# Kernel optimization log

Measured on AMD Instinct MI355X. Metric: run time of the kernel, lower is better.

Reference implementation:

```python
import jax, jax.numpy as jnp
import numpy as np


def _linear_interp(t, S):
    """1D linear interpolation along last axis, matching F.interpolate(mode='linear', align_corners=False).
    t: [B, C, L] -> [B, C, S]"""
    L = t.shape[-1]
    src = jnp.clip((jnp.arange(S, dtype=jnp.float32) + 0.5) * (L / S) - 0.5, 0.0, L - 1)
    i0 = jnp.floor(src).astype(jnp.int32)
    i1 = jnp.minimum(i0 + 1, L - 1)
    w = (src - i0.astype(jnp.float32)).astype(t.dtype)
    return t[..., i0] * (1.0 - w) + t[..., i1] * w


def setup_inputs() -> dict:
    key = jax.random.key(0)
    k1, k2, k3, k4 = jax.random.split(key, 4)
    B, C, H, W, L, D = 32, 768, 32, 32, 77, 512
    return {
        "img_feat": jax.random.normal(k1, (B, C, H, W), dtype=jnp.float32),
        "text_feat": jax.random.normal(k2, (B, L, D), dtype=jnp.float32),
        "W_txt": jax.random.normal(k3, (D, C), dtype=jnp.float32) / np.float32(np.sqrt(D)),
        "gamma": jax.random.normal(k4, (1,), dtype=jnp.float32) * 0.1,
    }


def reference(img_feat, text_feat, W_txt, gamma):
    B, C, H, W = img_feat.shape
    S = H * W
    q = img_feat.reshape(B, C, S)                          # [B,C,S]
    # Linear(D->C, bias=False) then transpose(1,2): [B,L,D] -> [B,C,L]
    t = jnp.einsum('bld,dc->bcl', text_feat, W_txt)
    t = _linear_interp(t, S)                               # [B,C,S]
    scale = S ** (-0.5)
    # attn = bmm(q [B,C,S], t^T [B,S,C]) * scale -> [B,C,C] channel attention
    attn = jax.nn.softmax(jnp.einsum('bis,bjs->bij', q, t) * scale, axis=-1)
    out = q + gamma * jnp.einsum('bij,bjs->bis', attn, t)  # gamma-gated residual
    return out.reshape(B, C, H, W)
```

## Files before the change

kernel.cpp:

```cpp
#include <hip/hip_runtime.h>

#define BB 32
#define CC 768
#define SS 1024
#define LLn 77
#define DD 512
#define LP 80
#define LP2 96

#define RATIO 0.0751953125f
#define IRATIO 13.298701f

#define CVT_TXT_BLOCKS (BB * LP * DD / 4 / 256)
#define CVT_W_BLOCKS ((CC / 32) * (DD / 32))
#define TG_BLOCKS (BB * 5 * 4)
#define QH_BLOCKS (256 * BB)

typedef short bf16x8 __attribute__((ext_vector_type(8)));
typedef float f32x4 __attribute__((ext_vector_type(4)));
typedef unsigned short u16;

__device__ __forceinline__ u16 f2bf(float f) {
    unsigned int u; __builtin_memcpy(&u, &f, 4);
    u += 0x7fffu + ((u >> 16) & 1u);
    return (u16)(u >> 16);
}

__global__ __launch_bounds__(256) void k_cvt(const float* __restrict__ text,
                                             const float* __restrict__ Wt,
                                             u16* __restrict__ At,
                                             u16* __restrict__ Wb) {
    __shared__ float tile[32 * 33];
    const int bx = blockIdx.x;
    const int tid = threadIdx.x;
    if (bx < CVT_TXT_BLOCKS) {
        int j = bx * 256 + tid;
        int row80 = j >> 7, col4 = (j & 127) << 2;
        int b = row80 / LP, l = row80 - b * LP;
        u16 o[4] = {0, 0, 0, 0};
        if (l < LLn) {
            float4 v = *reinterpret_cast<const float4*>(&text[((size_t)b * LLn + l) * DD + col4]);
            o[0] = f2bf(v.x); o[1] = f2bf(v.y); o[2] = f2bf(v.z); o[3] = f2bf(v.w);
        }
        *reinterpret_cast<uint2*>(&At[(size_t)row80 * DD + col4]) = *reinterpret_cast<uint2*>(o);
    } else {
        const int bw = bx - CVT_TXT_BLOCKS;
        const int c0 = (bw % (CC / 32)) * 32, d0 = (bw / (CC / 32)) * 32;
        const int tx = tid & 31, ty = tid >> 5;
#pragma unroll
        for (int k = 0; k < 4; ++k) {
            int d = ty + k * 8;
            tile[d * 33 + tx] = Wt[(size_t)(d0 + d) * CC + c0 + tx];
        }
        __syncthreads();
#pragma unroll
        for (int k = 0; k < 4; ++k) {
            int c = ty + k * 8;
            Wb[(size_t)(c0 + c) * DD + d0 + tx] = f2bf(tile[tx * 33 + c]);
        }
    }
}

__global__ __launch_bounds__(256) void k_mid(const float* __restrict__ q,
                                             const u16* __restrict__ At,
                                             const u16* __restrict__ Wb,
                                             u16* __restrict__ qh,
                                             u16* __restrict__ tc,
                                             u16* __restrict__ tlc) {
    __shared__ float smem[3 * 1024];
    const int bx = blockIdx.x;
    const int tid = threadIdx.x;

    if (bx < TG_BLOCKS) {
        const int cg = bx / 160, mt = bx % 160;
        const int b = mt / 5, tile = mt % 5;
        const int l0 = tile * 16;
        const int w = tid >> 6, lane = tid & 63;
        const int lm = lane & 15, lg = lane >> 4;
        const int c0 = cg * 192 + w * 48;

        f32x4 acc[3];
#pragma unroll
        for (int nt = 0; nt < 3; ++nt) acc[nt] = (f32x4){0.f, 0.f, 0.f, 0.f};

        const u16* ap = At + ((size_t)b * LP + l0 + lm) * DD + lg * 8;
        const u16* bp = Wb + (size_t)(c0 + lm) * DD + lg * 8;
#pragma unroll 4
        for (int ks = 0; ks < 16; ++ks) {
            bf16x8 aq = *reinterpret_cast<const bf16x8*>(ap + ks * 32);
#pragma unroll
            for (int nt = 0; nt < 3; ++nt) {
                bf16x8 bv = *reinterpret_cast<const bf16x8*>(bp + (size_t)nt * 16 * DD + ks * 32);
                acc[nt] = __builtin_amdgcn_mfma_f32_16x16x32_bf16(aq, bv, acc[nt], 0, 0, 0);
            }
        }

        const int lq = l0 + lg * 4;
#pragma unroll
        for (int nt = 0; nt < 3; ++nt) {
            int c = c0 + nt * 16 + lm;
            u16 pk[4];
#pragma unroll
            for (int r = 0; r < 4; ++r) pk[r] = f2bf(acc[nt][r]);
            uint2 pv; __builtin_memcpy(&pv, pk, 8);
            *reinterpret_cast<uint2*>(&tc[((size_t)b * CC + c) * LP2 + lq]) = pv;
#pragma unroll
            for (int r = 0; r < 4; ++r)
                tlc[((size_t)b * LP + lq + r) * CC + c] = pk[r];
        }
        if (tile == 4 && lg == 0) {
            uint4 z = {0u, 0u, 0u, 0u};
#pragma unroll
            for (int nt = 0; nt < 3; ++nt) {
                int c = c0 + nt * 16 + lm;
                *reinterpret_cast<uint4*>(&tc[((size_t)b * CC + c) * LP2 + 80]) = z;
                *reinterpret_cast<uint4*>(&tc[((size_t)b * CC + c) * LP2 + 88]) = z;
            }
        }
    } else {
        const int bxq = bx - TG_BLOCKS;
        const int b = bxq >> 8;
        const int c0 = (bxq & 255) * 3;
        for (int i4 = tid; i4 < 3 * 256; i4 += 256) {
            int r = i4 >> 8, col = (i4 & 255) << 2;
            *reinterpret_cast<float4*>(&smem[r * 1024 + col]) =
                *reinterpret_cast<const float4*>(&q[((size_t)b * CC + c0 + r) * SS + col]);
        }
        __syncthreads();
        for (int idx = tid; idx < 3 * LP2; idx += 256) {
            int r = idx / LP2, l = idx % LP2;
            float val = 0.f;
            if (l < LLn) {
                int s_lo = max(0, (int)floorf(((float)l - 0.5f) * IRATIO - 0.5f) - 1);
                int s_hi = min(SS - 1, (int)ceilf(((float)l + 1.5f) * IRATIO - 0.5f) + 1);
                float fl = (float)l;
                float a = 0.f;
                for (int s = s_lo; s <= s_hi; ++s) {
                    float src = fmaf((float)s + 0.5f, RATIO, -0.5f);
                    src = fminf(fmaxf(src, 0.f), 76.f);
                    float wgt = fmaxf(0.f, 1.f - fabsf(src - fl));
                    a = fmaf(wgt, smem[r * 1024 + s], a);
                }
                val = a * 0.03125f;
            }
            qh[((size_t)b * CC + c0 + r) * LP2 + l] = f2bf(val);
        }
    }
}

__global__ __launch_bounds__(256, 2) void k_attn_out(const u16* __restrict__ qh,
                                                     const u16* __restrict__ tc,
                                                     const u16* __restrict__ tlc,
                                                     const float* __restrict__ q,
                                                     const float* __restrict__ gamma,
                                                     float* __restrict__ out) {
    __shared__ float pmax[4][16];
    __shared__ float psum[4][16];
    __shared__ float us[16 * 80];
    __shared__ __align__(16) char pbuf[4][6400];

    const int b = blockIdx.y;
    const int iBase = blockIdx.x * 16;
    const int tid = threadIdx.x;
    const int w = tid >> 6, lane = tid & 63;
    const int lm = lane & 15, lg = lane >> 4;
    const float g = gamma[0];

    const u16* qbase = qh + ((size_t)b * CC + iBase + lm) * LP2 + lg * 8;
    bf16x8 aq0 = *reinterpret_cast<const bf16x8*>(qbase);
    bf16x8 aq1 = *reinterpret_cast<const bf16x8*>(qbase + 32);
    bf16x8 aq2 = *reinterpret_cast<const bf16x8*>(qbase + 64);

    f32x4 acc[12];
#pragma unroll
    for (int t = 0; t < 12; ++t) acc[t] = (f32x4){0.f, 0.f, 0.f, 0.f};

    const u16* tcb = tc + ((size_t)b * CC + w * 192 + lm) * LP2 + lg * 8;
#pragma unroll
    for (int t = 0; t < 12; ++t) {
        const u16* p = tcb + (size_t)t * 16 * LP2;
        bf16x8 b0 = *reinterpret_cast<const bf16x8*>(p);
        bf16x8 b1 = *reinterpret_cast<const bf16x8*>(p + 32);
        bf16x8 b2 = *reinterpret_cast<const bf16x8*>(p + 64);
        acc[t] = __builtin_amdgcn_mfma_f32_16x16x32_bf16(aq0, b0, acc[t], 0, 0, 0);
        acc[t] = __builtin_amdgcn_mfma_f32_16x16x32_bf16(aq1, b1, acc[t], 0, 0, 0);
        acc[t] = __builtin_amdgcn_mfma_f32_16x16x32_bf16(aq2, b2, acc[t], 0, 0, 0);
    }

    const size_t qBase = ((size_t)b * CC + iBase) * SS + (size_t)(tid << 2);
    f32x4 qreg[16];
#pragma unroll
    for (int r = 0; r < 16; ++r)
        qreg[r] = *reinterpret_cast<const f32x4*>(&q[qBase + (size_t)r * SS]);

    float m[4];
#pragma unroll
    for (int r = 0; r < 4; ++r) {
        float mm = acc[0][r];
#pragma unroll
        for (int t = 1; t < 12; ++t) mm = fmaxf(mm, acc[t][r]);
#pragma unroll
        for (int off = 8; off >= 1; off >>= 1) mm = fmaxf(mm, __shfl_xor(mm, off));
        m[r] = mm;
    }
    if (lm == 0) {
#pragma unroll
        for (int r = 0; r < 4; ++r) pmax[w][lg * 4 + r] = m[r];
    }
    __syncthreads();
    float gm[4];
#pragma unroll
    for (int r = 0; r < 4; ++r) {
        int row = lg * 4 + r;
        gm[r] = fmaxf(fmaxf(pmax[0][row], pmax[1][row]), fmaxf(pmax[2][row], pmax[3][row]));
    }
    float s[4] = {0.f, 0.f, 0.f, 0.f};
#pragma unroll
    for (int t = 0; t < 12; ++t) {
#pragma unroll
        for (int r = 0; r < 4; ++r) {
            float e = __expf(acc[t][r] - gm[r]);
            acc[t][r] = e;
            s[r] += e;
        }
    }
#pragma unroll
    for (int r = 0; r < 4; ++r) {
#pragma unroll
        for (int off = 8; off >= 1; off >>= 1) s[r] += __shfl_xor(s[r], off);
    }
    if (lm == 0) {
#pragma unroll
        for (int r = 0; r < 4; ++r) psum[w][lg * 4 + r] = s[r];
    }

    u16* P = (u16*)pbuf[w];
#pragma unroll
    for (int t = 0; t < 12; ++t) {
#pragma unroll
        for (int r = 0; r < 4; ++r)
            P[(lg * 4 + r) * 200 + t * 16 + lm] = f2bf(acc[t][r]);
    }

    f32x4 u[5];
#pragma unroll
    for (int nt = 0; nt < 5; ++nt) u[nt] = (f32x4){0.f, 0.f, 0.f, 0.f};
    const u16* tb = tlc + ((size_t)b * LP + lm) * CC + w * 192 + lg * 8;
#pragma unroll
    for (int ks = 0; ks < 6; ++ks) {
        bf16x8 pa = *reinterpret_cast<const bf16x8*>(&P[lm * 200 + ks * 32 + lg * 8]);
#pragma unroll
        for (int nt = 0; nt < 5; ++nt) {
            bf16x8 bv = *reinterpret_cast<const bf16x8*>(tb + (size_t)nt * 16 * CC + ks * 32);
            u[nt] = __builtin_amdgcn_mfma_f32_16x16x32_bf16(pa, bv, u[nt], 0, 0, 0);
        }
    }

    float* up = (float*)pbuf[w];
#pragma unroll
    for (int nt = 0; nt < 5; ++nt) {
#pragma unroll
        for (int r = 0; r < 4; ++r)
            up[(lg * 4 + r) * 81 + nt * 16 + lm] = u[nt][r];
    }
    __syncthreads();
#pragma unroll
    for (int k = 0; k < 5; ++k) {
        int idx = tid + (k << 8);
        int row = idx / LP, l = idx % LP;
        float v = ((float*)pbuf[0])[row * 81 + l] + ((float*)pbuf[1])[row * 81 + l]
                + ((float*)pbuf[2])[row * 81 + l] + ((float*)pbuf[3])[row * 81 + l];
        float denom = psum[0][row] + psum[1][row] + psum[2][row] + psum[3][row];
        us[row * LP + l] = v / denom;
    }
    __syncthreads();

    const int s0 = tid << 2;
    int i0x[4], i1x[4];
    float wx[4];
#pragma unroll
    for (int k = 0; k < 4; ++k) {
        float src = fmaf((float)(s0 + k) + 0.5f, RATIO, -0.5f);
        src = fminf(fmaxf(src, 0.f), 76.f);
        i0x[k] = (int)src;
        wx[k] = src - (float)i0x[k];
        i1x[k] = (i0x[k] < 76) ? i0x[k] + 1 : 76;
    }
#pragma unroll
    for (int r = 0; r < 16; ++r) {
        const float* ur = &us[r * LP];
        f32x4 o;
#pragma unroll
        for (int k = 0; k < 4; ++k) {
            float uv = fmaf(1.f - wx[k], ur[i0x[k]], wx[k] * ur[i1x[k]]);
            o[k] = qreg[r][k] + g * uv;
        }
        __builtin_nontemporal_store(o, reinterpret_cast<f32x4*>(&out[qBase + (size_t)r * SS]));
    }
}

extern "C" void kernel_launch(void* const* d_in, const int* in_sizes, int n_in,
                              void* d_out, int out_size, void* d_ws, size_t ws_size,
                              hipStream_t stream) {
    const float* img   = (const float*)d_in[0];
    const float* text  = (const float*)d_in[1];
    const float* Wt    = (const float*)d_in[2];
    const float* gamma = (const float*)d_in[3];
    float* out = (float*)d_out;
    char* ws = (char*)d_ws;
    u16*   tc_bf  = (u16*)(ws);
    u16*   tlc_bf = (u16*)(ws + 4718592);
    u16*   qh_bf  = (u16*)(ws + 8650752);
    u16*   At_bf  = (u16*)(ws + 13369344);
    u16*   Wb_bf  = (u16*)(ws + 15990784);

    k_cvt<<<dim3(CVT_TXT_BLOCKS + CVT_W_BLOCKS), 256, 0, stream>>>(text, Wt, At_bf, Wb_bf);
    k_mid<<<dim3(TG_BLOCKS + QH_BLOCKS), 256, 0, stream>>>(img, At_bf, Wb_bf, qh_bf, tc_bf, tlc_bf);
    k_attn_out<<<dim3(48, BB), 256, 0, stream>>>(qh_bf, tc_bf, tlc_bf, img, gamma, out);
}
```

Before: 100.3 us.

## Fuse q-side interpolation reduction into attention kernel, dropping separate qh pass

The projection of q onto the 77 text positions (the transpose of the linear interpolation) is now computed inside the attention kernel from the q rows it already loads, using shared-memory atomic accumulation, instead of a separate pass over all of img_feat in the middle kernel. This removes one full read of the 100MB input and the qh round trip through global memory. In exchange it adds shared-memory atomics and extra syncs before the MFMA stage, and the q register loads now come before the score computation.

```diff
diff --git a/kernel.cpp b/kernel.cpp
--- a/kernel.cpp
+++ b/kernel.cpp
@@ -9,12 +9,10 @@
 #define LP2 96
 
 #define RATIO 0.0751953125f
-#define IRATIO 13.298701f
 
 #define CVT_TXT_BLOCKS (BB * LP * DD / 4 / 256)
 #define CVT_W_BLOCKS ((CC / 32) * (DD / 32))
 #define TG_BLOCKS (BB * 5 * 4)
-#define QH_BLOCKS (256 * BB)
 
 typedef short bf16x8 __attribute__((ext_vector_type(8)));
 typedef float f32x4 __attribute__((ext_vector_type(4)));
@@ -61,101 +59,68 @@
     }
 }
 
-__global__ __launch_bounds__(256) void k_mid(const float* __restrict__ q,
-                                             const u16* __restrict__ At,
-                                             const u16* __restrict__ Wb,
-                                             u16* __restrict__ qh,
-                                             u16* __restrict__ tc,
-                                             u16* __restrict__ tlc) {
-    __shared__ float smem[3 * 1024];
+__global__ __launch_bounds__(256) void k_tgemm(const u16* __restrict__ At,
+                                               const u16* __restrict__ Wb,
+                                               u16* __restrict__ tc,
+                                               u16* __restrict__ tlc) {
     const int bx = blockIdx.x;
     const int tid = threadIdx.x;
-
-    if (bx < TG_BLOCKS) {
-        const int cg = bx / 160, mt = bx % 160;
-        const int b = mt / 5, tile = mt % 5;
-        const int l0 = tile * 16;
-        const int w = tid >> 6, lane = tid & 63;
-        const int lm = lane & 15, lg = lane >> 4;
-        const int c0 = cg * 192 + w * 48;
-
-        f32x4 acc[3];
-#pragma unroll
-        for (int nt = 0; nt < 3; ++nt) acc[nt] = (f32x4){0.f, 0.f, 0.f, 0.f};
-
-        const u16* ap = At + ((size_t)b * LP + l0 + lm) * DD + lg * 8;
-        const u16* bp = Wb + (size_t)(c0 + lm) * DD + lg * 8;
+    const int cg = bx / 160, mt = bx % 160;
+    const int b = mt / 5, tile = mt % 5;
+    const int l0 = tile * 16;
+    const int w = tid >> 6, lane = tid & 63;
+    const int lm = lane & 15, lg = lane >> 4;
+    const int c0 = cg * 192 + w * 48;
+
+    f32x4 acc[3];
+#pragma unroll
+    for (int nt = 0; nt < 3; ++nt) acc[nt] = (f32x4){0.f, 0.f, 0.f, 0.f};
+
+    const u16* ap = At + ((size_t)b * LP + l0 + lm) * DD + lg * 8;
+    const u16* bp = Wb + (size_t)(c0 + lm) * DD + lg * 8;
 #pragma unroll 4
-        for (int ks = 0; ks < 16; ++ks) {
-            bf16x8 aq = *reinterpret_cast<const bf16x8*>(ap + ks * 32);
-#pragma unroll
-            for (int nt = 0; nt < 3; ++nt) {
-                bf16x8 bv = *reinterpret_cast<const bf16x8*>(bp + (size_t)nt * 16 * DD + ks * 32);
-                acc[nt] = __builtin_amdgcn_mfma_f32_16x16x32_bf16(aq, bv, acc[nt], 0, 0, 0);
-            }
-        }
-
-        const int lq = l0 + lg * 4;
+    for (int ks = 0; ks < 16; ++ks) {
+        bf16x8 aq = *reinterpret_cast<const bf16x8*>(ap + ks * 32);
+#pragma unroll
+        for (int nt = 0; nt < 3; ++nt) {
+            bf16x8 bv = *reinterpret_cast<const bf16x8*>(bp + (size_t)nt * 16 * DD + ks * 32);
+            acc[nt] = __builtin_amdgcn_mfma_f32_16x16x32_bf16(aq, bv, acc[nt], 0, 0, 0);
+        }
+    }
+
+    const int lq = l0 + lg * 4;
+#pragma unroll
+    for (int nt = 0; nt < 3; ++nt) {
+        int c = c0 + nt * 16 + lm;
+        u16 pk[4];
+#pragma unroll
+        for (int r = 0; r < 4; ++r) pk[r] = f2bf(acc[nt][r]);
+        uint2 pv; __builtin_memcpy(&pv, pk, 8);
+        *reinterpret_cast<uint2*>(&tc[((size_t)b * CC + c) * LP2 + lq]) = pv;
+#pragma unroll
+        for (int r = 0; r < 4; ++r)
+            tlc[((size_t)b * LP + lq + r) * CC + c] = pk[r];
+    }
+    if (tile == 4 && lg == 0) {
+        uint4 z = {0u, 0u, 0u, 0u};
 #pragma unroll
         for (int nt = 0; nt < 3; ++nt) {
             int c = c0 + nt * 16 + lm;
-            u16 pk[4];
-#pragma unroll
-            for (int r = 0; r < 4; ++r) pk[r] = f2bf(acc[nt][r]);
-            uint2 pv; __builtin_memcpy(&pv, pk, 8);
-            *reinterpret_cast<uint2*>(&tc[((size_t)b * CC + c) * LP2 + lq]) = pv;
-#pragma unroll
-            for (int r = 0; r < 4; ++r)
-                tlc[((size_t)b * LP + lq + r) * CC + c] = pk[r];
-        }
-        if (tile == 4 && lg == 0) {
-            uint4 z = {0u, 0u, 0u, 0u};
-#pragma unroll
-            for (int nt = 0; nt < 3; ++nt) {
-                int c = c0 + nt * 16 + lm;
-                *reinterpret_cast<uint4*>(&tc[((size_t)b * CC + c) * LP2 + 80]) = z;
-                *reinterpret_cast<uint4*>(&tc[((size_t)b * CC + c) * LP2 + 88]) = z;
-            }
-        }
-    } else {
-        const int bxq = bx - TG_BLOCKS;
-        const int b = bxq >> 8;
-        const int c0 = (bxq & 255) * 3;
-        for (int i4 = tid; i4 < 3 * 256; i4 += 256) {
-            int r = i4 >> 8, col = (i4 & 255) << 2;
-            *reinterpret_cast<float4*>(&smem[r * 1024 + col]) =
-                *reinterpret_cast<const float4*>(&q[((size_t)b * CC + c0 + r) * SS + col]);
-        }
-        __syncthreads();
-        for (int idx = tid; idx < 3 * LP2; idx += 256) {
-            int r = idx / LP2, l = idx % LP2;
-            float val = 0.f;
-            if (l < LLn) {
-                int s_lo = max(0, (int)floorf(((float)l - 0.5f) * IRATIO - 0.5f) - 1);
-                int s_hi = min(SS - 1, (int)ceilf(((float)l + 1.5f) * IRATIO - 0.5f) + 1);
-                float fl = (float)l;
-                float a = 0.f;
-                for (int s = s_lo; s <= s_hi; ++s) {
-                    float src = fmaf((float)s + 0.5f, RATIO, -0.5f);
-                    src = fminf(fmaxf(src, 0.f), 76.f);
-                    float wgt = fmaxf(0.f, 1.f - fabsf(src - fl));
-                    a = fmaf(wgt, smem[r * 1024 + s], a);
-                }
-                val = a * 0.03125f;
-            }
-            qh[((size_t)b * CC + c0 + r) * LP2 + l] = f2bf(val);
-        }
-    }
-}
-
-__global__ __launch_bounds__(256, 2) void k_attn_out(const u16* __restrict__ qh,
-                                                     const u16* __restrict__ tc,
-                                                     const u16* __restrict__ tlc,
-                                                     const float* __restrict__ q,
-                                                     const float* __restrict__ gamma,
-                                                     float* __restrict__ out) {
+            *reinterpret_cast<uint4*>(&tc[((size_t)b * CC + c) * LP2 + 80]) = z;
+            *reinterpret_cast<uint4*>(&tc[((size_t)b * CC + c) * LP2 + 88]) = z;
+        }
+    }
+}
+
+__global__ __launch_bounds__(256, 2) void k_fused(const u16* __restrict__ tc,
+                                                  const u16* __restrict__ tlc,
+                                                  const float* __restrict__ q,
+                                                  const float* __restrict__ gamma,
+                                                  float* __restrict__ out) {
     __shared__ float pmax[4][16];
     __shared__ float psum[4][16];
+    __shared__ float qh_f32[16 * 80];
+    __shared__ u16 qh_bf[16 * 96];
     __shared__ float us[16 * 80];
     __shared__ __align__(16) char pbuf[4][6400];
 
@@ -166,10 +131,53 @@
     const int lm = lane & 15, lg = lane >> 4;
     const float g = gamma[0];
 
-    const u16* qbase = qh + ((size_t)b * CC + iBase + lm) * LP2 + lg * 8;
-    bf16x8 aq0 = *reinterpret_cast<const bf16x8*>(qbase);
-    bf16x8 aq1 = *reinterpret_cast<const bf16x8*>(qbase + 32);
-    bf16x8 aq2 = *reinterpret_cast<const bf16x8*>(qbase + 64);
+    const size_t qBase = ((size_t)b * CC + iBase) * SS + (size_t)(tid << 2);
+    f32x4 qreg[16];
+#pragma unroll
+    for (int r = 0; r < 16; ++r)
+        qreg[r] = *reinterpret_cast<const f32x4*>(&q[qBase + (size_t)r * SS]);
+
+    for (int i = tid; i < 16 * 80; i += 256) qh_f32[i] = 0.f;
+    __syncthreads();
+
+    const int s0 = tid << 2;
+    float wgt[4]; int i0k[4];
+#pragma unroll
+    for (int k = 0; k < 4; ++k) {
+        float src = fmaf((float)(s0 + k) + 0.5f, RATIO, -0.5f);
+        src = fminf(fmaxf(src, 0.f), 76.f);
+        i0k[k] = (int)src;
+        wgt[k] = src - (float)i0k[k];
+    }
+    const int la = i0k[0];
+#pragma unroll
+    for (int r = 0; r < 16; ++r) {
+        float c0 = 0.f, c1 = 0.f, c2 = 0.f;
+#pragma unroll
+        for (int k = 0; k < 4; ++k) {
+            float qv = qreg[r][k];
+            bool hi = (i0k[k] != la);
+            float a0 = (1.f - wgt[k]) * qv, a1 = wgt[k] * qv;
+            c0 += hi ? 0.f : a0;
+            c1 += hi ? a0 : a1;
+            c2 += hi ? a1 : 0.f;
+        }
+        atomicAdd(&qh_f32[r * 80 + la], c0);
+        atomicAdd(&qh_f32[r * 80 + la + 1], c1);
+        if (c2 != 0.f) atomicAdd(&qh_f32[r * 80 + la + 2], c2);
+    }
+    __syncthreads();
+
+    for (int i = tid; i < 16 * 96; i += 256) {
+        int row = i / 96, col = i - row * 96;
+        float v = (col < LLn) ? qh_f32[row * 80 + col] * 0.03125f : 0.f;
+        qh_bf[i] = f2bf(v);
+    }
+    __syncthreads();
+
+    bf16x8 aq0 = *reinterpret_cast<const bf16x8*>(&qh_bf[lm * 96 + lg * 8]);
+    bf16x8 aq1 = *reinterpret_cast<const bf16x8*>(&qh_bf[lm * 96 + 32 + lg * 8]);
+    bf16x8 aq2 = *reinterpret_cast<const bf16x8*>(&qh_bf[lm * 96 + 64 + lg * 8]);
 
     f32x4 acc[12];
 #pragma unroll
@@ -187,12 +195,6 @@
         acc[t] = __builtin_amdgcn_mfma_f32_16x16x32_bf16(aq2, b2, acc[t], 0, 0, 0);
     }
 
-    const size_t qBase = ((size_t)b * CC + iBase) * SS + (size_t)(tid << 2);
-    f32x4 qreg[16];
-#pragma unroll
-    for (int r = 0; r < 16; ++r)
-        qreg[r] = *reinterpret_cast<const f32x4*>(&q[qBase + (size_t)r * SS]);
-
     float m[4];
 #pragma unroll
     for (int r = 0; r < 4; ++r) {
@@ -275,24 +277,16 @@
     }
     __syncthreads();
 
-    const int s0 = tid << 2;
-    int i0x[4], i1x[4];
-    float wx[4];
-#pragma unroll
-    for (int k = 0; k < 4; ++k) {
-        float src = fmaf((float)(s0 + k) + 0.5f, RATIO, -0.5f);
-        src = fminf(fmaxf(src, 0.f), 76.f);
-        i0x[k] = (int)src;
-        wx[k] = src - (float)i0x[k];
-        i1x[k] = (i0x[k] < 76) ? i0x[k] + 1 : 76;
-    }
+    int i1x[4];
+#pragma unroll
+    for (int k = 0; k < 4; ++k) i1x[k] = (i0k[k] < 76) ? i0k[k] + 1 : 76;
 #pragma unroll
     for (int r = 0; r < 16; ++r) {
         const float* ur = &us[r * LP];
         f32x4 o;
 #pragma unroll
         for (int k = 0; k < 4; ++k) {
-            float uv = fmaf(1.f - wx[k], ur[i0x[k]], wx[k] * ur[i1x[k]]);
+            float uv = fmaf(1.f - wgt[k], ur[i0k[k]], wgt[k] * ur[i1x[k]]);
             o[k] = qreg[r][k] + g * uv;
         }
         __builtin_nontemporal_store(o, reinterpret_cast<f32x4*>(&out[qBase + (size_t)r * SS]));
@@ -310,11 +304,10 @@
     char* ws = (char*)d_ws;
     u16*   tc_bf  = (u16*)(ws);
     u16*   tlc_bf = (u16*)(ws + 4718592);
-    u16*   qh_bf  = (u16*)(ws + 8650752);
-    u16*   At_bf  = (u16*)(ws + 13369344);
-    u16*   Wb_bf  = (u16*)(ws + 15990784);
+    u16*   At_bf  = (u16*)(ws + 8650752);
+    u16*   Wb_bf  = (u16*)(ws + 11272192);
 
     k_cvt<<<dim3(CVT_TXT_BLOCKS + CVT_W_BLOCKS), 256, 0, stream>>>(text, Wt, At_bf, Wb_bf);
-    k_mid<<<dim3(TG_BLOCKS + QH_BLOCKS), 256, 0, stream>>>(img, At_bf, Wb_bf, qh_bf, tc_bf, tlc_bf);
-    k_attn_out<<<dim3(48, BB), 256, 0, stream>>>(qh_bf, tc_bf, tlc_bf, img, gamma, out);
-}
+    k_tgemm<<<dim3(TG_BLOCKS), 256, 0, stream>>>(At_bf, Wb_bf, tc_bf, tlc_bf);
+    k_fused<<<dim3(48, BB), 256, 0, stream>>>(tc_bf, tlc_bf, img, gamma, out);
+}
```

After: 168.8 us. +68.3%, slower.

## Rebalance kernel stages and remap attention blocks across batches

Applied to the files above, without the earlier changes.

Moves the q-downsampling work (qh) out of the middle kernel into the first prep kernel alongside the text/weight conversions. This leaves a small dedicated text-GEMM kernel and makes the large q-read pass independent of the GEMM. The attention kernel switches to a 1D grid whose block ids are swizzled so consecutive blocks cover eight different batches, changing which blocks share cache and which XCD each lands on. The risk is that the prep kernel grows and the text GEMM becomes a small, underfilled launch of its own.

```diff
diff --git a/kernel.cpp b/kernel.cpp
--- a/kernel.cpp
+++ b/kernel.cpp
@@ -13,26 +13,34 @@
 
 #define CVT_TXT_BLOCKS (BB * LP * DD / 4 / 256)
 #define CVT_W_BLOCKS ((CC / 32) * (DD / 32))
+#define QH_BLOCKS (256 * BB)
+#define PREP_BLOCKS (CVT_TXT_BLOCKS + CVT_W_BLOCKS + QH_BLOCKS)
 #define TG_BLOCKS (BB * 5 * 4)
-#define QH_BLOCKS (256 * BB)
+#define ATTN_BLOCKS (48 * BB)
 
 typedef short bf16x8 __attribute__((ext_vector_type(8)));
 typedef float f32x4 __attribute__((ext_vector_type(4)));
 typedef unsigned short u16;
+typedef unsigned int u32;
+
+#define MFMA __builtin_amdgcn_mfma_f32_16x16x32_bf16
 
 __device__ __forceinline__ u16 f2bf(float f) {
-    unsigned int u; __builtin_memcpy(&u, &f, 4);
+    u32 u; __builtin_memcpy(&u, &f, 4);
     u += 0x7fffu + ((u >> 16) & 1u);
     return (u16)(u >> 16);
 }
 
-__global__ __launch_bounds__(256) void k_cvt(const float* __restrict__ text,
-                                             const float* __restrict__ Wt,
-                                             u16* __restrict__ At,
-                                             u16* __restrict__ Wb) {
-    __shared__ float tile[32 * 33];
+__global__ __launch_bounds__(256) void k_prep(const float* __restrict__ q,
+                                              const float* __restrict__ text,
+                                              const float* __restrict__ Wt,
+                                              u16* __restrict__ At,
+                                              u16* __restrict__ Wb,
+                                              u16* __restrict__ qh) {
+    __shared__ float smem[3 * 1024];
     const int bx = blockIdx.x;
     const int tid = threadIdx.x;
+
     if (bx < CVT_TXT_BLOCKS) {
         int j = bx * 256 + tid;
         int row80 = j >> 7, col4 = (j & 127) << 2;
@@ -43,10 +51,11 @@
             o[0] = f2bf(v.x); o[1] = f2bf(v.y); o[2] = f2bf(v.z); o[3] = f2bf(v.w);
         }
         *reinterpret_cast<uint2*>(&At[(size_t)row80 * DD + col4]) = *reinterpret_cast<uint2*>(o);
-    } else {
+    } else if (bx < CVT_TXT_BLOCKS + CVT_W_BLOCKS) {
         const int bw = bx - CVT_TXT_BLOCKS;
         const int c0 = (bw % (CC / 32)) * 32, d0 = (bw / (CC / 32)) * 32;
         const int tx = tid & 31, ty = tid >> 5;
+        float* tile = smem;
 #pragma unroll
         for (int k = 0; k < 4; ++k) {
             int d = ty + k * 8;
@@ -58,67 +67,8 @@
             int c = ty + k * 8;
             Wb[(size_t)(c0 + c) * DD + d0 + tx] = f2bf(tile[tx * 33 + c]);
         }
-    }
-}
-
-__global__ __launch_bounds__(256) void k_mid(const float* __restrict__ q,
-                                             const u16* __restrict__ At,
-                                             const u16* __restrict__ Wb,
-                                             u16* __restrict__ qh,
-                                             u16* __restrict__ tc,
-                                             u16* __restrict__ tlc) {
-    __shared__ float smem[3 * 1024];
-    const int bx = blockIdx.x;
-    const int tid = threadIdx.x;
-
-    if (bx < TG_BLOCKS) {
-        const int cg = bx / 160, mt = bx % 160;
-        const int b = mt / 5, tile = mt % 5;
-        const int l0 = tile * 16;
-        const int w = tid >> 6, lane = tid & 63;
-        const int lm = lane & 15, lg = lane >> 4;
-        const int c0 = cg * 192 + w * 48;
-
-        f32x4 acc[3];
-#pragma unroll
-        for (int nt = 0; nt < 3; ++nt) acc[nt] = (f32x4){0.f, 0.f, 0.f, 0.f};
-
-        const u16* ap = At + ((size_t)b * LP + l0 + lm) * DD + lg * 8;
-        const u16* bp = Wb + (size_t)(c0 + lm) * DD + lg * 8;
-#pragma unroll 4
-        for (int ks = 0; ks < 16; ++ks) {
-            bf16x8 aq = *reinterpret_cast<const bf16x8*>(ap + ks * 32);
-#pragma unroll
-            for (int nt = 0; nt < 3; ++nt) {
-                bf16x8 bv = *reinterpret_cast<const bf16x8*>(bp + (size_t)nt * 16 * DD + ks * 32);
-                acc[nt] = __builtin_amdgcn_mfma_f32_16x16x32_bf16(aq, bv, acc[nt], 0, 0, 0);
-            }
-        }
-
-        const int lq = l0 + lg * 4;
-#pragma unroll
-        for (int nt = 0; nt < 3; ++nt) {
-            int c = c0 + nt * 16 + lm;
-            u16 pk[4];
-#pragma unroll
-            for (int r = 0; r < 4; ++r) pk[r] = f2bf(acc[nt][r]);
-            uint2 pv; __builtin_memcpy(&pv, pk, 8);
-            *reinterpret_cast<uint2*>(&tc[((size_t)b * CC + c) * LP2 + lq]) = pv;
-#pragma unroll
-            for (int r = 0; r < 4; ++r)
-                tlc[((size_t)b * LP + lq + r) * CC + c] = pk[r];
-        }
-        if (tile == 4 && lg == 0) {
-            uint4 z = {0u, 0u, 0u, 0u};
-#pragma unroll
-            for (int nt = 0; nt < 3; ++nt) {
-                int c = c0 + nt * 16 + lm;
-                *reinterpret_cast<uint4*>(&tc[((size_t)b * CC + c) * LP2 + 80]) = z;
-                *reinterpret_cast<uint4*>(&tc[((size_t)b * CC + c) * LP2 + 88]) = z;
-            }
-        }
     } else {
-        const int bxq = bx - TG_BLOCKS;
+        const int bxq = bx - CVT_TXT_BLOCKS - CVT_W_BLOCKS;
         const int b = bxq >> 8;
         const int c0 = (bxq & 255) * 3;
         for (int i4 = tid; i4 < 3 * 256; i4 += 256) {
@@ -148,6 +98,59 @@
     }
 }
 
+__global__ __launch_bounds__(256) void k_tgemm(const u16* __restrict__ At,
+                                               const u16* __restrict__ Wb,
+                                               u16* __restrict__ tc,
+                                               u16* __restrict__ tlc) {
+    const int bx = blockIdx.x;
+    const int tid = threadIdx.x;
+    const int cg = bx / 160, mt = bx % 160;
+    const int b = mt / 5, tile = mt % 5;
+    const int l0 = tile * 16;
+    const int w = tid >> 6, lane = tid & 63;
+    const int lm = lane & 15, lg = lane >> 4;
+    const int c0 = cg * 192 + w * 48;
+
+    f32x4 acc[3];
+#pragma unroll
+    for (int nt = 0; nt < 3; ++nt) acc[nt] = (f32x4){0.f, 0.f, 0.f, 0.f};
+
+    const u16* ap = At + ((size_t)b * LP + l0 + lm) * DD + lg * 8;
+    const u16* bp = Wb + (size_t)(c0 + lm) * DD + lg * 8;
+#pragma unroll 4
+    for (int ks = 0; ks < 16; ++ks) {
+        bf16x8 aq = *reinterpret_cast<const bf16x8*>(ap + ks * 32);
+#pragma unroll
+        for (int nt = 0; nt < 3; ++nt) {
+            bf16x8 bv = *reinterpret_cast<const bf16x8*>(bp + (size_t)nt * 16 * DD + ks * 32);
+            acc[nt] = MFMA(aq, bv, acc[nt], 0, 0, 0);
+        }
+    }
+
+    const int lq = l0 + lg * 4;
+#pragma unroll
+    for (int nt = 0; nt < 3; ++nt) {
+        int c = c0 + nt * 16 + lm;
+        u16 pk[4];
+#pragma unroll
+        for (int r = 0; r < 4; ++r) pk[r] = f2bf(acc[nt][r]);
+        uint2 pv; __builtin_memcpy(&pv, pk, 8);
+        *reinterpret_cast<uint2*>(&tc[((size_t)b * CC + c) * LP2 + lq]) = pv;
+#pragma unroll
+        for (int r = 0; r < 4; ++r)
+            tlc[((size_t)b * LP + lq + r) * CC + c] = pk[r];
+    }
+    if (tile == 4 && lg == 0) {
+        uint4 z = {0u, 0u, 0u, 0u};
+#pragma unroll
+        for (int nt = 0; nt < 3; ++nt) {
+            int c = c0 + nt * 16 + lm;
+            *reinterpret_cast<uint4*>(&tc[((size_t)b * CC + c) * LP2 + 80]) = z;
+            *reinterpret_cast<uint4*>(&tc[((size_t)b * CC + c) * LP2 + 88]) = z;
+        }
+    }
+}
+
 __global__ __launch_bounds__(256, 2) void k_attn_out(const u16* __restrict__ qh,
                                                      const u16* __restrict__ tc,
                                                      const u16* __restrict__ tlc,
@@ -159,8 +162,10 @@
     __shared__ float us[16 * 80];
     __shared__ __align__(16) char pbuf[4][6400];
 
-    const int b = blockIdx.y;
-    const int iBase = blockIdx.x * 16;
+    const int id = blockIdx.x;
+    const int o = id >> 3;
+    const int b = (id & 7) * 4 + o / 48;
+    const int iBase = (o % 48) * 16;
     const int tid = threadIdx.x;
     const int w = tid >> 6, lane = tid & 63;
     const int lm = lane & 15, lg = lane >> 4;
@@ -182,9 +187,9 @@
         bf16x8 b0 = *reinterpret_cast<const bf16x8*>(p);
         bf16x8 b1 = *reinterpret_cast<const bf16x8*>(p + 32);
         bf16x8 b2 = *reinterpret_cast<const bf16x8*>(p + 64);
-        acc[t] = __builtin_amdgcn_mfma_f32_16x16x32_bf16(aq0, b0, acc[t], 0, 0, 0);
-        acc[t] = __builtin_amdgcn_mfma_f32_16x16x32_bf16(aq1, b1, acc[t], 0, 0, 0);
-        acc[t] = __builtin_amdgcn_mfma_f32_16x16x32_bf16(aq2, b2, acc[t], 0, 0, 0);
+        acc[t] = MFMA(aq0, b0, acc[t], 0, 0, 0);
+        acc[t] = MFMA(aq1, b1, acc[t], 0, 0, 0);
+        acc[t] = MFMA(aq2, b2, acc[t], 0, 0, 0);
     }
 
     const size_t qBase = ((size_t)b * CC + iBase) * SS + (size_t)(tid << 2);
@@ -252,7 +257,7 @@
 #pragma unroll
         for (int nt = 0; nt < 5; ++nt) {
             bf16x8 bv = *reinterpret_cast<const bf16x8*>(tb + (size_t)nt * 16 * CC + ks * 32);
-            u[nt] = __builtin_amdgcn_mfma_f32_16x16x32_bf16(pa, bv, u[nt], 0, 0, 0);
+            u[nt] = MFMA(pa, bv, u[nt], 0, 0, 0);
         }
     }
 
@@ -267,7 +272,7 @@
 #pragma unroll
     for (int k = 0; k < 5; ++k) {
         int idx = tid + (k << 8);
-        int row = idx / LP, l = idx % LP;
+        int row = idx / LP, l = idx - row * LP;
         float v = ((float*)pbuf[0])[row * 81 + l] + ((float*)pbuf[1])[row * 81 + l]
                 + ((float*)pbuf[2])[row * 81 + l] + ((float*)pbuf[3])[row * 81 + l];
         float denom = psum[0][row] + psum[1][row] + psum[2][row] + psum[3][row];
@@ -276,26 +281,25 @@
     __syncthreads();
 
     const int s0 = tid << 2;
-    int i0x[4], i1x[4];
-    float wx[4];
+    float wgt[4]; int i0k[4], i1x[4];
 #pragma unroll
     for (int k = 0; k < 4; ++k) {
         float src = fmaf((float)(s0 + k) + 0.5f, RATIO, -0.5f);
         src = fminf(fmaxf(src, 0.f), 76.f);
-        i0x[k] = (int)src;
-        wx[k] = src - (float)i0x[k];
-        i1x[k] = (i0x[k] < 76) ? i0x[k] + 1 : 76;
+        i0k[k] = (int)src;
+        wgt[k] = src - (float)i0k[k];
+        i1x[k] = (i0k[k] < 76) ? i0k[k] + 1 : 76;
     }
 #pragma unroll
     for (int r = 0; r < 16; ++r) {
         const float* ur = &us[r * LP];
-        f32x4 o;
+        f32x4 ov;
 #pragma unroll
         for (int k = 0; k < 4; ++k) {
-            float uv = fmaf(1.f - wx[k], ur[i0x[k]], wx[k] * ur[i1x[k]]);
-            o[k] = qreg[r][k] + g * uv;
-        }
-        __builtin_nontemporal_store(o, reinterpret_cast<f32x4*>(&out[qBase + (size_t)r * SS]));
+            float uv = fmaf(1.f - wgt[k], ur[i0k[k]], wgt[k] * ur[i1x[k]]);
+            ov[k] = qreg[r][k] + g * uv;
+        }
+        __builtin_nontemporal_store(ov, reinterpret_cast<f32x4*>(&out[qBase + (size_t)r * SS]));
     }
 }
 
@@ -314,7 +318,7 @@
     u16*   At_bf  = (u16*)(ws + 13369344);
     u16*   Wb_bf  = (u16*)(ws + 15990784);
 
-    k_cvt<<<dim3(CVT_TXT_BLOCKS + CVT_W_BLOCKS), 256, 0, stream>>>(text, Wt, At_bf, Wb_bf);
-    k_mid<<<dim3(TG_BLOCKS + QH_BLOCKS), 256, 0, stream>>>(img, At_bf, Wb_bf, qh_bf, tc_bf, tlc_bf);
-    k_attn_out<<<dim3(48, BB), 256, 0, stream>>>(qh_bf, tc_bf, tlc_bf, img, gamma, out);
-}
+    k_prep<<<dim3(PREP_BLOCKS), 256, 0, stream>>>(img, text, Wt, At_bf, Wb_bf, qh_bf);
+    k_tgemm<<<dim3(TG_BLOCKS), 256, 0, stream>>>(At_bf, Wb_bf, tc_bf, tlc_bf);
+    k_attn_out<<<dim3(ATTN_BLOCKS), 256, 0, stream>>>(qh_bf, tc_bf, tlc_bf, img, gamma, out);
+}
```

Result: slower. 105.1 us (+4.7%).
